# Kernel optimization log

Hardware: AMD Instinct MI355X
Metric: run time of the kernel (lower is better)

## Reference

```python
import jax, jax.numpy as jnp
import numpy as np

B, C, H, W = 64, 128, 56, 56
ALPHA = 0.001


def _build_inhi_mat(out_channels):
    # Circulant 0/1 band: row i has ones at columns (i-r//2 ... i+r//2) mod C,
    # exactly matching the torch double loop with modular wrap-around.
    r = out_channels // 8 + 1  # inhiRange
    i = np.arange(out_channels)[:, None]
    d = np.arange(-(r // 2), r // 2 + 1)[None, :]
    cols = (i + d) % out_channels  # [C, r]
    m = np.zeros((out_channels, out_channels), dtype=np.float32)
    m[np.repeat(i, d.shape[1], axis=1), cols] = 1.0
    return m


def setup_inputs() -> dict:
    key = jax.random.key(0)
    x = jax.random.normal(key, (B, C, H, W), dtype=jnp.float32)
    inhiMat = jnp.asarray(_build_inhi_mat(C))  # [C, C] constant buffer
    return {"x": x, "inhiMat": inhiMat}


def reference(x, inhiMat):
    b, c, h, w = x.shape
    inhiRange = c // 8 + 1
    # y = detach(x)^2 -> banded cross-channel sum (bmm with broadcast [C,C] mat)
    y = jax.lax.stop_gradient(x) ** 2
    y = y.reshape(b, c, h * w)
    y = jnp.einsum('ij,bjs->bis', inhiMat, y)  # same math as bmm with tiled inhi
    y = y.reshape(b, c, h, w)
    denom = (y * ALPHA / inhiRange + 1.0) ** 0.75
    return x / denom
```

## Files before the change

kernel.cpp:

```cpp
#include <hip/hip_runtime.h>


#define B_DIM 64
#define C_DIM 128
#define HW_DIM (56 * 56)
#define HW4 (HW_DIM / 4)
#define NCOL4 (B_DIM * HW4)
#define CH 8
#define PLANES (CH + 16)

__device__ __forceinline__ float pow_m075(float t) {
    return __builtin_amdgcn_exp2f(-0.75f * __builtin_amdgcn_logf(t));
}

__global__ __launch_bounds__(64, 4) void lrn_kernel(const float4* __restrict__ x,
                                                    float4* __restrict__ out) {
    const float kAlphaOverR = 0.001f / 17.0f;

    const int col4 = blockIdx.x * 64 + threadIdx.x;
    const int b    = col4 / HW4;
    const int hw4  = col4 - b * HW4;
    const int c0   = blockIdx.y * CH;

    const float4* base = x + ((size_t)b * C_DIM) * HW4 + hw4;
    float4* obase      = out + ((size_t)b * C_DIM) * HW4 + hw4;

    float4 v[PLANES];
#pragma unroll
    for (int j = 0; j < PLANES; ++j) {
        const int ch = (c0 + j - 8 + C_DIM) & (C_DIM - 1);
        v[j] = base[(size_t)ch * HW4];
    }

    float sx = 0.f, sy = 0.f, sz = 0.f, sw = 0.f;
#pragma unroll
    for (int j = 0; j < 17; ++j) {
        sx = fmaf(v[j].x, v[j].x, sx);
        sy = fmaf(v[j].y, v[j].y, sy);
        sz = fmaf(v[j].z, v[j].z, sz);
        sw = fmaf(v[j].w, v[j].w, sw);
    }

#pragma unroll
    for (int i = 0; i < CH; ++i) {
        const float4 xc = v[8 + i];
        float4 o;
        o.x = xc.x * pow_m075(fmaf(sx, kAlphaOverR, 1.0f));
        o.y = xc.y * pow_m075(fmaf(sy, kAlphaOverR, 1.0f));
        o.z = xc.z * pow_m075(fmaf(sz, kAlphaOverR, 1.0f));
        o.w = xc.w * pow_m075(fmaf(sw, kAlphaOverR, 1.0f));
        obase[(size_t)(c0 + i) * HW4] = o;

        if (i < CH - 1) {
            const float4 a = v[17 + i];
            const float4 d = v[i];
            sx += a.x * a.x - d.x * d.x;
            sy += a.y * a.y - d.y * d.y;
            sz += a.z * a.z - d.z * d.z;
            sw += a.w * a.w - d.w * d.w;
        }
    }
}

extern "C" void kernel_launch(void* const* d_in, const int* in_sizes, int n_in,
                              void* d_out, int out_size, void* d_ws, size_t ws_size,
                              hipStream_t stream) {
    const float4* x = (const float4*)d_in[0];
    float4* out = (float4*)d_out;

    dim3 grid(NCOL4 / 64, C_DIM / CH);
    lrn_kernel<<<grid, 64, 0, stream>>>(x, out);
}
```

Measured before the change: 187.3 us.

## Stream channel planes through an LDS ring with async global-to-LDS loads

Each block now covers 64 channels instead of 8. Input planes are streamed into a 26-slot shared-memory ring using global_load_lds, with hand-placed vmcnt waits that keep about 16 loads in flight. This cuts the halo re-read overhead, which drops from 3x redundant reads to 1.25x, and overlaps loads with compute. The cost is fragile manual wait counting, a larger LDS footprint, far fewer blocks in the channel dimension, and possible hazards when ring slots are reused.

```diff
diff --git a/kernel.cpp b/kernel.cpp
--- a/kernel.cpp
+++ b/kernel.cpp
@@ -1,59 +1,73 @@
 #include <hip/hip_runtime.h>
 
 
-#define B_DIM 64
-#define C_DIM 128
-#define HW_DIM (56 * 56)
-#define HW4 (HW_DIM / 4)
-#define NCOL4 (B_DIM * HW4)
-#define CH 8
-#define PLANES (CH + 16)
+#define HW4 784
+#define BSTR (128 * HW4)
+#define NCOL4 (64 * HW4)
+#define SEGC 64
+#define RING 26
+#define DQ 16
+
+typedef __attribute__((address_space(3))) unsigned int lds_u32;
+typedef __attribute__((address_space(1))) const unsigned int glb_u32;
 
 __device__ __forceinline__ float pow_m075(float t) {
     return __builtin_amdgcn_exp2f(-0.75f * __builtin_amdgcn_logf(t));
 }
 
-__global__ __launch_bounds__(64, 4) void lrn_kernel(const float4* __restrict__ x,
-                                                    float4* __restrict__ out) {
+__global__ __launch_bounds__(64) void lrn_kernel(const float4* __restrict__ x,
+                                                 float4* __restrict__ out) {
     const float kAlphaOverR = 0.001f / 17.0f;
 
-    const int col4 = blockIdx.x * 64 + threadIdx.x;
+    __shared__ float4 ring[RING][64];
+
+    const int lane = threadIdx.x;
+    const int col4 = blockIdx.x * 64 + lane;
     const int b    = col4 / HW4;
     const int hw4  = col4 - b * HW4;
-    const int c0   = blockIdx.y * CH;
+    const int c0   = blockIdx.y * SEGC;
 
-    const float4* base = x + ((size_t)b * C_DIM) * HW4 + hw4;
-    float4* obase      = out + ((size_t)b * C_DIM) * HW4 + hw4;
+    const float4* bx = x + (size_t)b * BSTR + hw4;
+    float4*       bo = out + (size_t)b * BSTR + hw4;
 
-    float4 v[PLANES];
 #pragma unroll
-    for (int j = 0; j < PLANES; ++j) {
-        const int ch = (c0 + j - 8 + C_DIM) & (C_DIM - 1);
-        v[j] = base[(size_t)ch * HW4];
+    for (int p = -8; p < DQ; ++p) {
+        const int ch = (c0 + p) & 127;
+        __builtin_amdgcn_global_load_lds((glb_u32*)(bx + (size_t)ch * HW4),
+                                         (lds_u32*)&ring[p + 8][0], 16, 0, 0);
     }
+    asm volatile("s_waitcnt vmcnt(7)" ::: "memory");
 
     float sx = 0.f, sy = 0.f, sz = 0.f, sw = 0.f;
 #pragma unroll
     for (int j = 0; j < 17; ++j) {
-        sx = fmaf(v[j].x, v[j].x, sx);
-        sy = fmaf(v[j].y, v[j].y, sy);
-        sz = fmaf(v[j].z, v[j].z, sz);
-        sw = fmaf(v[j].w, v[j].w, sw);
+        const float4 v = ring[j][lane];
+        sx = fmaf(v.x, v.x, sx);
+        sy = fmaf(v.y, v.y, sy);
+        sz = fmaf(v.z, v.z, sz);
+        sw = fmaf(v.w, v.w, sw);
     }
 
 #pragma unroll
-    for (int i = 0; i < CH; ++i) {
-        const float4 xc = v[8 + i];
+    for (int c = 0; c < SEGC; ++c) {
+        const int pl = (c + DQ <= SEGC + 7) ? (c + DQ) : (SEGC + 7);
+        const int ch = (c0 + pl) & 127;
+        __builtin_amdgcn_global_load_lds((glb_u32*)(bx + (size_t)ch * HW4),
+                                         (lds_u32*)&ring[(pl + 8) % RING][0], 16, 0, 0);
+
+        const float4 xc = ring[(c + 8) % RING][lane];
         float4 o;
         o.x = xc.x * pow_m075(fmaf(sx, kAlphaOverR, 1.0f));
         o.y = xc.y * pow_m075(fmaf(sy, kAlphaOverR, 1.0f));
         o.z = xc.z * pow_m075(fmaf(sz, kAlphaOverR, 1.0f));
         o.w = xc.w * pow_m075(fmaf(sw, kAlphaOverR, 1.0f));
-        obase[(size_t)(c0 + i) * HW4] = o;
+        bo[(size_t)(c0 + c) * HW4] = o;
 
-        if (i < CH - 1) {
-            const float4 a = v[17 + i];
-            const float4 d = v[i];
+        if (c < SEGC - 1) {
+            if (c < 7) asm volatile("s_waitcnt vmcnt(8)" ::: "memory");
+            else       asm volatile("s_waitcnt vmcnt(15)" ::: "memory");
+            const float4 a = ring[(c + 17) % RING][lane];
+            const float4 d = ring[c % RING][lane];
             sx += a.x * a.x - d.x * d.x;
             sy += a.y * a.y - d.y * d.y;
             sz += a.z * a.z - d.z * d.z;
@@ -68,6 +82,6 @@
     const float4* x = (const float4*)d_in[0];
     float4* out = (float4*)d_out;
 
-    dim3 grid(NCOL4 / 64, C_DIM / CH);
+    dim3 grid(NCOL4 / 64, 128 / SEGC);
     lrn_kernel<<<grid, 64, 0, stream>>>(x, out);
 }
```

New measurement: 221.1 us. 1.18x slower.
